# Kernel tuning notes

Hardware: AMD Instinct MI355X
Metric: run time of the kernel (lower is better)

## Reference

```python
import jax, jax.numpy as jnp
import numpy as np

B, D, T, H, F, O, S = 256, 128, 64, 256, 16, 1, 1
TWO_PI = 2.0 * np.pi


def hsig(x):
    # torch.nn.Hardsigmoid: clip(x/6 + 0.5, 0, 1)
    return jnp.clip(x / 6.0 + 0.5, 0.0, 1.0)


def sfm_forward(input_x, W_i, U_i, b_i, W_ste, U_ste, b_ste, W_fre, U_fre, b_fre,
                W_c, U_c, b_c, W_o, U_o, b_o, U_a, b_a, W_p, b_p, fc_w, fc_b):
    # [B, D*T] -> [B, D, T] -> [B, T, D] -> time-major [T, B, D]
    x = input_x.reshape(B, D, T).transpose(0, 2, 1)
    xs = x.transpose(1, 0, 2)
    freq = jnp.arange(F, dtype=jnp.float32) / F          # [F]
    times = jnp.arange(1, T + 1, dtype=jnp.float32)      # time counter per step

    h0 = jnp.zeros((B, H), jnp.float32)
    S0 = jnp.zeros((B, H, F), jnp.float32)

    def step(carry, inps):
        h, S_re, S_im = carry
        xt, t = inps  # xt: [B, D], t: scalar
        x_i = xt @ W_i + b_i
        x_ste = xt @ W_ste + b_ste
        x_fre = xt @ W_fre + b_fre
        x_c = xt @ W_c + b_c
        x_o = xt @ W_o + b_o
        i = hsig(x_i + h @ U_i)                       # [B, H]
        ste = hsig(x_ste + h @ U_ste)                 # [B, H]
        fre = hsig(x_fre + h @ U_fre)                 # [B, F]
        f = ste[:, :, None] * fre[:, None, :]         # [B, H, F]
        c = i * jnp.tanh(x_c + h @ U_c)               # [B, H]
        omega = TWO_PI * t * freq                     # [F]
        re = jnp.cos(omega)
        im = jnp.sin(omega)
        S_re = f * S_re + c[:, :, None] * re          # [B, H, F]
        S_im = f * S_im + c[:, :, None] * im
        A = S_re * S_re + S_im * S_im                 # [B, H, F]
        A_a = jnp.einsum('bhf,f->bh', A, U_a[:, 0])   # (B*H, F) @ (F, 1) reshaped
        a = jnp.tanh(A_a + b_a)
        o = hsig(x_o + h @ U_o)
        h_new = o * a
        return (h_new, S_re, S_im), None

    (h, _, _), _ = jax.lax.scan(step, (h0, S0, S0), (xs, times))
    p = h @ W_p + b_p                                 # [B, O*S]
    return p @ fc_w.T + fc_b                          # [B, S]


def setup_inputs() -> dict:
    key = jax.random.key(0)
    ks = jax.random.split(key, 16)
    g = lambda k, sh: jax.random.normal(k, sh, jnp.float32) * 0.05
    inp = {
        'input_x': jax.random.normal(ks[0], (B, D * T), jnp.float32),
        'W_i': g(ks[1], (D, H)), 'U_i': g(ks[2], (H, H)), 'b_i': jnp.zeros((H,), jnp.float32),
        'W_ste': g(ks[3], (D, H)), 'U_ste': g(ks[4], (H, H)), 'b_ste': jnp.ones((H,), jnp.float32),
        'W_fre': g(ks[5], (D, F)), 'U_fre': g(ks[6], (H, F)), 'b_fre': jnp.ones((F,), jnp.float32),
        'W_c': g(ks[7], (D, H)), 'U_c': g(ks[8], (H, H)), 'b_c': jnp.zeros((H,), jnp.float32),
        'W_o': g(ks[9], (D, H)), 'U_o': g(ks[10], (H, H)), 'b_o': jnp.zeros((H,), jnp.float32),
        'U_a': g(ks[11], (F, 1)), 'b_a': jnp.zeros((H,), jnp.float32),
        'W_p': g(ks[12], (H, O * S)), 'b_p': jnp.zeros((O * S,), jnp.float32),
        'fc_w': g(ks[13], (S, O * S)), 'fc_b': jnp.zeros((S,), jnp.float32),
    }
    return inp


def reference(input_x, W_i, U_i, b_i, W_ste, U_ste, b_ste, W_fre, U_fre, b_fre,
              W_c, U_c, b_c, W_o, U_o, b_o, U_a, b_a, W_p, b_p, fc_w, fc_b):
    return sfm_forward(input_x, W_i, U_i, b_i, W_ste, U_ste, b_ste, W_fre, U_fre, b_fre,
                       W_c, U_c, b_c, W_o, U_o, b_o, U_a, b_a, W_p, b_p, fc_w, fc_b)
```

## Files before the change

### kernel.cpp

```cpp
#include <hip/hip_runtime.h>
#include <hip/hip_bf16.h>
#include <hip/hip_fp16.h>
#include <math.h>

#define B_ 256
#define D_ 128
#define T_ 64
#define H_ 256
#define F_ 16
#define GCOLS 1024

#define XPG_OFF 0
#define XPF_OFF 67108864
#define UPK_OFF 67633152

__device__ __forceinline__ float hsig(float x) {
    return fminf(fmaxf(fmaf(x, 0.16666667f, 0.5f), 0.0f), 1.0f);
}

__global__ __launch_bounds__(256) void xproj_kernel(
    const float* __restrict__ input_x,
    const float* __restrict__ W_i,   const float* __restrict__ b_i,
    const float* __restrict__ W_ste, const float* __restrict__ b_ste,
    const float* __restrict__ W_c,   const float* __restrict__ b_c,
    const float* __restrict__ W_o,   const float* __restrict__ b_o,
    const float* __restrict__ W_fre, const float* __restrict__ b_fre,
    float* __restrict__ xpg, __half* __restrict__ xpf)
{
    __shared__ float xt[16][128];
    const int tid = threadIdx.x;
    const int bx  = blockIdx.x;
    const int t   = bx >> 4;
    const int bg  = bx & 15;

    for (int i = tid; i < 16 * 128; i += 256) {
        int r = i >> 7, d = i & 127;
        xt[r][d] = input_x[(size_t)(bg * 16 + r) * (D_ * T_) + (d << 6) + t];
    }
    __syncthreads();

    const int j  = tid;
    const int jf = j & 15;

    float acc[16][4];
#pragma unroll
    for (int r = 0; r < 16; r++) { acc[r][0] = 0.f; acc[r][1] = 0.f; acc[r][2] = 0.f; acc[r][3] = 0.f; }
    float accf[16];
#pragma unroll
    for (int r = 0; r < 16; r++) accf[r] = 0.f;

    for (int d = 0; d < 128; d++) {
        float w0 = W_i  [d * 256 + j];
        float w1 = W_ste[d * 256 + j];
        float w2 = W_c  [d * 256 + j];
        float w3 = W_o  [d * 256 + j];
        float wf = W_fre[d * 16 + jf];
#pragma unroll
        for (int r = 0; r < 16; r++) {
            float xv = xt[r][d];
            acc[r][0] = fmaf(xv, w0, acc[r][0]);
            acc[r][1] = fmaf(xv, w1, acc[r][1]);
            acc[r][2] = fmaf(xv, w2, acc[r][2]);
            acc[r][3] = fmaf(xv, w3, acc[r][3]);
            accf[r]   = fmaf(xv, wf, accf[r]);
        }
    }

    const float bi = b_i[j], bs = b_ste[j], bc = b_c[j], bo = b_o[j];
    const float bf = b_fre[jf];
    const size_t row0 = (size_t)t * B_ + (size_t)bg * 16;
#pragma unroll
    for (int r = 0; r < 16; r++) {
        const size_t row = row0 + r;
        float4 v = make_float4(acc[r][0] + bi, acc[r][1] + bs,
                               acc[r][2] + bc, acc[r][3] + bo);
        *(float4*)(xpg + row * GCOLS + (j << 2)) = v;
        if (j < 16) xpf[row * 16 + j] = __float2half(accf[r] + bf);
    }
}

__global__ __launch_bounds__(256) void pack_kernel(
    const float* __restrict__ U_i, const float* __restrict__ U_ste,
    const float* __restrict__ U_c, const float* __restrict__ U_o,
    __half* __restrict__ Upk)
{
    const int k = blockIdx.x, j = threadIdx.x;
    const int idx = (k << 8) + j;
    __half* dst = Upk + ((size_t)idx << 2);
    dst[0] = __float2half(U_i  [idx]);
    dst[1] = __float2half(U_ste[idx]);
    dst[2] = __float2half(U_c  [idx]);
    dst[3] = __float2half(U_o  [idx]);
}

__global__ __launch_bounds__(512) void scan_kernel(
    const float* __restrict__ xpg, const __half* __restrict__ xpf,
    const __half* __restrict__ Upk,
    const float* __restrict__ U_fre,
    const float* __restrict__ U_a, const float* __restrict__ b_a,
    const float* __restrict__ W_p, const float* __restrict__ b_p,
    const float* __restrict__ fc_w, const float* __restrict__ fc_b,
    float* __restrict__ out)
{
    __shared__ float h_lds[256];
    __shared__ float fre_w[256 * 16];
    __shared__ float red5[5][256];
    __shared__ float fre_lds[16];
    __shared__ float tabc[16], tabs[16];

    const int tid  = threadIdx.x;
    const int j    = tid & 255;
    const int half = tid >> 8;
    const int kbase = half << 7;
    const int b    = blockIdx.x;
    const int jf   = j & 15;

    if (tid < 256) h_lds[tid] = 0.0f;
    if (tid < 16) {
        tabc[tid] = cosf((float)(M_PI / 8.0) * (float)tid);
        tabs[tid] = sinf((float)(M_PI / 8.0) * (float)tid);
    }
    for (int i = tid; i < 256 * 16; i += 512)
        fre_w[i] = U_fre[i];

    float Sre[16], Sim[16];
#pragma unroll
    for (int f = 0; f < 16; f++) { Sre[f] = 0.f; Sim[f] = 0.f; }
    float ua[16];
#pragma unroll
    for (int f = 0; f < 16; f++) ua[f] = U_a[f];
    const float ba = b_a[j];
    __syncthreads();

    for (int t = 0; t < T_; t++) {
        const size_t row = (size_t)t * B_ + b;

        float x_i = 0.f, x_s = 0.f, x_c = 0.f, x_o = 0.f, x_f = 0.f;
        if (half == 0) {
            float4 xv = *(const float4*)(xpg + row * GCOLS + (j << 2));
            x_i = xv.x; x_s = xv.y; x_c = xv.z; x_o = xv.w;
            x_f = __half2float(xpf[row * 16 + jf]);
        }

        float a0 = 0.f, a1 = 0.f, a2 = 0.f, a3 = 0.f, af = 0.f;
#pragma unroll 8
        for (int kk = 0; kk < 128; kk++) {
            const int k = kbase + kk;
            const float hk = h_lds[k];
            union { uint2 u; __half2 h2[2]; } w;
            w.u = *(const uint2*)(Upk + ((((size_t)k << 8) + j) << 2));
            a0 = fmaf(__low2float (w.h2[0]), hk, a0);
            a1 = fmaf(__high2float(w.h2[0]), hk, a1);
            a2 = fmaf(__low2float (w.h2[1]), hk, a2);
            a3 = fmaf(__high2float(w.h2[1]), hk, a3);
            af = fmaf(fre_w[(k << 4) + jf],  hk, af);
        }

        if (half == 1) {
            red5[0][j] = a0; red5[1][j] = a1; red5[2][j] = a2;
            red5[3][j] = a3; red5[4][j] = af;
        }
        __syncthreads();

        float gs = 0.f, cc = 0.f, go = 0.f;
        if (half == 0) {
            a0 += red5[0][j]; a1 += red5[1][j]; a2 += red5[2][j];
            a3 += red5[3][j]; af += red5[4][j];
            float gi = hsig(x_i + a0);
            gs = hsig(x_s + a1);
            cc = gi * tanhf(x_c + a2);
            go = hsig(x_o + a3);
            float gf = hsig(x_f + af);
            if (j < 16) fre_lds[j] = gf;
        }
        __syncthreads();

        if (half == 0) {
            const int tp = t + 1;
            float accA = 0.f;
#pragma unroll
            for (int f = 0; f < 16; f++) {
                int m = (tp * f) & 15;
                float re = tabc[m], im = tabs[m];
                float ff = gs * fre_lds[f];
                Sre[f] = ff * Sre[f] + cc * re;
                Sim[f] = ff * Sim[f] + cc * im;
                float Af = fmaf(Sre[f], Sre[f], Sim[f] * Sim[f]);
                accA = fmaf(Af, ua[f], accA);
            }
            float a    = tanhf(accA + ba);
            h_lds[j]   = go * a;
        }
        __syncthreads();
    }

    float* redf = &red5[0][0];
    if (half == 0) redf[j] = h_lds[j] * W_p[j];
    __syncthreads();
    for (int s = 128; s > 0; s >>= 1) {
        if (half == 0 && j < s) redf[j] += redf[j + s];
        __syncthreads();
    }
    if (tid == 0) out[b] = (redf[0] + b_p[0]) * fc_w[0] + fc_b[0];
}

extern "C" void kernel_launch(void* const* d_in, const int* in_sizes, int n_in,
                              void* d_out, int out_size, void* d_ws, size_t ws_size,
                              hipStream_t stream) {
    const float* input_x = (const float*)d_in[0];
    const float* W_i   = (const float*)d_in[1];
    const float* U_i   = (const float*)d_in[2];
    const float* b_i   = (const float*)d_in[3];
    const float* W_ste = (const float*)d_in[4];
    const float* U_ste = (const float*)d_in[5];
    const float* b_ste = (const float*)d_in[6];
    const float* W_fre = (const float*)d_in[7];
    const float* U_fre = (const float*)d_in[8];
    const float* b_fre = (const float*)d_in[9];
    const float* W_c   = (const float*)d_in[10];
    const float* U_c   = (const float*)d_in[11];
    const float* b_c   = (const float*)d_in[12];
    const float* W_o   = (const float*)d_in[13];
    const float* U_o   = (const float*)d_in[14];
    const float* b_o   = (const float*)d_in[15];
    const float* U_a   = (const float*)d_in[16];
    const float* b_a   = (const float*)d_in[17];
    const float* W_p   = (const float*)d_in[18];
    const float* b_p   = (const float*)d_in[19];
    const float* fc_w  = (const float*)d_in[20];
    const float* fc_b  = (const float*)d_in[21];

    char* ws = (char*)d_ws;
    float*  xpg = (float*)(ws + XPG_OFF);
    __half* xpf = (__half*)(ws + XPF_OFF);
    __half* Upk = (__half*)(ws + UPK_OFF);
    float* out = (float*)d_out;

    pack_kernel<<<dim3(256), dim3(256), 0, stream>>>(U_i, U_ste, U_c, U_o, Upk);

    xproj_kernel<<<dim3(T_ * 16), dim3(256), 0, stream>>>(
        input_x, W_i, b_i, W_ste, b_ste, W_c, b_c, W_o, b_o, W_fre, b_fre,
        xpg, xpf);

    scan_kernel<<<dim3(B_), dim3(512), 0, stream>>>(
        xpg, xpf, Upk, U_fre, U_a, b_a, W_p, b_p, fc_w, fc_b, out);
}
```

Baseline: 713.6 us.

## Split scan recurrent matvec across four thread groups and drop one barrier

The scan kernel now runs 1024 threads per batch row, splitting the K=256 recurrent reduction into four 64-wide slices, with three partial-sum sets reduced through LDS. U_fre is transposed in shared memory so h and the fre weights are read as float4. The frequency gate is broadcast with a wavefront shuffle instead of an extra LDS round trip, which removes one __syncthreads per timestep. This shortens the serial per-step dot-product chain, at the cost of more reduction traffic and higher per-block thread and register pressure.

```diff
diff --git a/kernel.cpp b/kernel.cpp
--- a/kernel.cpp
+++ b/kernel.cpp
@@ -93,7 +93,7 @@
     dst[3] = __float2half(U_o  [idx]);
 }
 
-__global__ __launch_bounds__(512) void scan_kernel(
+__global__ __launch_bounds__(1024) void scan_kernel(
     const float* __restrict__ xpg, const __half* __restrict__ xpf,
     const __half* __restrict__ Upk,
     const float* __restrict__ U_fre,
@@ -103,25 +103,26 @@
     float* __restrict__ out)
 {
     __shared__ float h_lds[256];
-    __shared__ float fre_w[256 * 16];
-    __shared__ float red5[5][256];
-    __shared__ float fre_lds[16];
+    __shared__ float freT[16 * 256];
+    __shared__ float red[15][256];
     __shared__ float tabc[16], tabs[16];
 
-    const int tid  = threadIdx.x;
-    const int j    = tid & 255;
-    const int half = tid >> 8;
-    const int kbase = half << 7;
-    const int b    = blockIdx.x;
-    const int jf   = j & 15;
+    const int tid = threadIdx.x;
+    const int j   = tid & 255;
+    const int q   = tid >> 8;
+    const int kbase = q << 6;
+    const int b   = blockIdx.x;
+    const int jf  = j & 15;
 
     if (tid < 256) h_lds[tid] = 0.0f;
     if (tid < 16) {
         tabc[tid] = cosf((float)(M_PI / 8.0) * (float)tid);
         tabs[tid] = sinf((float)(M_PI / 8.0) * (float)tid);
     }
-    for (int i = tid; i < 256 * 16; i += 512)
-        fre_w[i] = U_fre[i];
+    for (int i = tid; i < 16 * 256; i += 1024) {
+        int f = i >> 8, k = i & 255;
+        freT[i] = U_fre[(k << 4) + f];
+    }
 
     float Sre[16], Sim[16];
 #pragma unroll
@@ -136,69 +137,75 @@
         const size_t row = (size_t)t * B_ + b;
 
         float x_i = 0.f, x_s = 0.f, x_c = 0.f, x_o = 0.f, x_f = 0.f;
-        if (half == 0) {
+        if (q == 0) {
             float4 xv = *(const float4*)(xpg + row * GCOLS + (j << 2));
             x_i = xv.x; x_s = xv.y; x_c = xv.z; x_o = xv.w;
             x_f = __half2float(xpf[row * 16 + jf]);
         }
 
         float a0 = 0.f, a1 = 0.f, a2 = 0.f, a3 = 0.f, af = 0.f;
-#pragma unroll 8
-        for (int kk = 0; kk < 128; kk++) {
+#pragma unroll 4
+        for (int kk = 0; kk < 64; kk += 4) {
             const int k = kbase + kk;
-            const float hk = h_lds[k];
-            union { uint2 u; __half2 h2[2]; } w;
-            w.u = *(const uint2*)(Upk + ((((size_t)k << 8) + j) << 2));
-            a0 = fmaf(__low2float (w.h2[0]), hk, a0);
-            a1 = fmaf(__high2float(w.h2[0]), hk, a1);
-            a2 = fmaf(__low2float (w.h2[1]), hk, a2);
-            a3 = fmaf(__high2float(w.h2[1]), hk, a3);
-            af = fmaf(fre_w[(k << 4) + jf],  hk, af);
-        }
-
-        if (half == 1) {
-            red5[0][j] = a0; red5[1][j] = a1; red5[2][j] = a2;
-            red5[3][j] = a3; red5[4][j] = af;
+            const float4 h4 = *(const float4*)&h_lds[k];
+            const float4 f4 = *(const float4*)&freT[(jf << 8) + k];
+#pragma unroll
+            for (int u = 0; u < 4; u++) {
+                union { uint2 uu; __half2 h2[2]; } w;
+                w.uu = *(const uint2*)(Upk + ((((size_t)(k + u)) << 8) + j) * 4);
+                const float hk = (&h4.x)[u];
+                a0 = fmaf(__low2float (w.h2[0]), hk, a0);
+                a1 = fmaf(__high2float(w.h2[0]), hk, a1);
+                a2 = fmaf(__low2float (w.h2[1]), hk, a2);
+                a3 = fmaf(__high2float(w.h2[1]), hk, a3);
+                af = fmaf((&f4.x)[u], hk, af);
+            }
+        }
+
+        if (q) {
+            const int base = (q - 1) * 5;
+            red[base + 0][j] = a0; red[base + 1][j] = a1; red[base + 2][j] = a2;
+            red[base + 3][j] = a3; red[base + 4][j] = af;
         }
         __syncthreads();
 
-        float gs = 0.f, cc = 0.f, go = 0.f;
-        if (half == 0) {
-            a0 += red5[0][j]; a1 += red5[1][j]; a2 += red5[2][j];
-            a3 += red5[3][j]; af += red5[4][j];
+        if (q == 0) {
+#pragma unroll
+            for (int qq = 0; qq < 3; qq++) {
+                a0 += red[qq * 5 + 0][j]; a1 += red[qq * 5 + 1][j];
+                a2 += red[qq * 5 + 2][j]; a3 += red[qq * 5 + 3][j];
+                af += red[qq * 5 + 4][j];
+            }
             float gi = hsig(x_i + a0);
-            gs = hsig(x_s + a1);
-            cc = gi * tanhf(x_c + a2);
-            go = hsig(x_o + a3);
+            float gs = hsig(x_s + a1);
+            float cc = gi * tanhf(x_c + a2);
+            float go = hsig(x_o + a3);
             float gf = hsig(x_f + af);
-            if (j < 16) fre_lds[j] = gf;
-        }
-        __syncthreads();
-
-        if (half == 0) {
+
             const int tp = t + 1;
             float accA = 0.f;
 #pragma unroll
             for (int f = 0; f < 16; f++) {
+                float fre_f = __shfl(gf, f);
                 int m = (tp * f) & 15;
                 float re = tabc[m], im = tabs[m];
-                float ff = gs * fre_lds[f];
+                float ff = gs * fre_f;
                 Sre[f] = ff * Sre[f] + cc * re;
                 Sim[f] = ff * Sim[f] + cc * im;
                 float Af = fmaf(Sre[f], Sre[f], Sim[f] * Sim[f]);
                 accA = fmaf(Af, ua[f], accA);
             }
-            float a    = tanhf(accA + ba);
-            h_lds[j]   = go * a;
+            float a  = tanhf(accA + ba);
+            h_lds[j] = go * a;
         }
         __syncthreads();
     }
 
-    float* redf = &red5[0][0];
-    if (half == 0) redf[j] = h_lds[j] * W_p[j];
+    float* redf = &red[0][0];
+    if (q == 0) redf[j] = h_lds[j] * W_p[j];
     __syncthreads();
     for (int s = 128; s > 0; s >>= 1) {
-        if (half == 0 && j < s) redf[j] += redf[j + s];
+        if (q == 0 && j < s) redf[j] += redf[j + s];
         __syncthreads();
     }
     if (tid == 0) out[b] = (redf[0] + b_p[0]) * fc_w[0] + fc_b[0];
@@ -242,6 +249,6 @@
         input_x, W_i, b_i, W_ste, b_ste, W_c, b_c, W_o, b_o, W_fre, b_fre,
         xpg, xpf);
 
-    scan_kernel<<<dim3(B_), dim3(512), 0, stream>>>(
+    scan_kernel<<<dim3(B_), dim3(1024), 0, stream>>>(
         xpg, xpf, Upk, U_fre, U_a, b_a, W_p, b_p, fc_w, fc_b, out);
 }
```

Result: slower. 818.1 us (+14.7%).
